# Performance work log

Hardware: AMD Instinct MI355X
Metric: run time of the kernel (lower is better)

The kernel has to match this reference:

```python
import jax, jax.numpy as jnp
import numpy as np

H, W = 300, 400            # grid_size
RES = 0.1                  # resolution (m/pixel)
X0, X1 = -20.0, 20.0       # x_range
Y0, Y1 = -10.0, 30.0       # y_range
Z0, Z1 = -3.0, 4.0         # z_range
MAX_INT = 255.0            # max_intensity
N_MAX = 128.0              # density_normalize
K_SAMPLES = 512            # >= max Bresenham steps inside grid (diag <= 400)


def _rasterize_polyline(pts_xy):
    """DDA line rasterization of an ego-frame polyline -> [H, W] binary grid.
    Matches the Bresenham + 3x3 stamp (width 2 or 3 -> half_w=1) of the original."""
    px = jnp.trunc((pts_xy[:, 0] - X0) / RES)  # int() truncation as in original
    py = jnp.trunc((pts_xy[:, 1] - Y0) / RES)
    p = jnp.stack([px, py], axis=-1)           # [N, 2] pixel coords (float)
    a, b = p[:-1], p[1:]                        # segment endpoints [S, 2]

    def inb(q):
        return (q[:, 0] >= 0) & (q[:, 0] < W) & (q[:, 1] >= 0) & (q[:, 1] < H)

    valid = inb(a) | inb(b)                     # draw if either endpoint in bounds
    lo = jnp.array([0.0, 0.0], jnp.float32)
    hi = jnp.array([W - 1.0, H - 1.0], jnp.float32)
    a = jnp.clip(a, lo, hi)
    b = jnp.clip(b, lo, hi)

    dmax = jnp.max(jnp.abs(b - a), axis=-1)     # [S] major-axis length in pixels
    k = jnp.arange(K_SAMPLES, dtype=jnp.float32)
    t = jnp.minimum(k[None, :], dmax[:, None]) / jnp.maximum(dmax[:, None], 1.0)
    pts = a[:, None, :] + t[..., None] * (b - a)[:, None, :]   # [S, K, 2]
    pix = jnp.round(pts).astype(jnp.int32)

    offs = jnp.arange(-1, 2)                    # half_w = width//2 = 1 -> 3x3 stamp
    xs = pix[..., 0][..., None, None] + offs[:, None]          # [S, K, 3, 1]
    ys = pix[..., 1][..., None, None] + offs[None, :]          # [S, K, 1, 3]
    xs, ys = jnp.broadcast_arrays(xs, ys)
    val = jnp.broadcast_to(valid.astype(jnp.float32)[:, None, None, None], xs.shape)
    # out-of-bounds stamped pixels are dropped, as in the original bounds check
    return jnp.zeros((H, W), jnp.float32).at[ys, xs].max(val, mode="drop")


def _rasterize_lidar(points):
    """[N,4] (x,y,z,intensity) -> [3,H,W] (height, mean intensity, log density)."""
    x, y, z, inten = points[:, 0], points[:, 1], points[:, 2], points[:, 3]
    mask = (x >= X0) & (x < X1) & (y >= Y0) & (y < Y1)
    px = jnp.clip(((x - X0) / RES).astype(jnp.int32), 0, W - 1)
    py = jnp.clip(((y - Y0) / RES).astype(jnp.int32), 0, H - 1)
    w = mask.astype(jnp.float32)
    neg_inf = jnp.float32(-jnp.inf)

    hmax = jnp.full((H, W), neg_inf, jnp.float32).at[py, px].max(
        jnp.where(mask, z, neg_inf))
    hmax = jnp.where(jnp.isneginf(hmax), 0.0, hmax)  # empty cells -> 0 BEFORE norm

    isum = jnp.zeros((H, W), jnp.float32).at[py, px].add(inten * w)
    cnt = jnp.zeros((H, W), jnp.float32).at[py, px].add(w)
    imean = jnp.where(cnt > 0, isum / jnp.maximum(cnt, 1.0), 0.0)

    h = jnp.clip((hmax - Z0) / (Z1 - Z0), 0.0, 1.0)
    i = jnp.clip(imean / MAX_INT, 0.0, 1.0)
    d = jnp.clip(jnp.log1p(cnt) / jnp.log(1.0 + N_MAX), 0.0, 1.0)
    return jnp.stack([h, i, d])


def setup_inputs() -> dict:
    key = jax.random.key(0)
    k1, k2 = jax.random.split(key)
    # LiDAR: 4M points, slightly wider than the ROI so ~some get filtered
    u = jax.random.uniform(k1, (4_000_000, 4), dtype=jnp.float32)
    lo = jnp.array([-25.0, -15.0, -3.0, 0.0], jnp.float32)
    hi = jnp.array([25.0, 35.0, 4.0, 255.0], jnp.float32)
    lidar_points = lo + u * (hi - lo)
    # trajectory: smooth forward path in ego frame
    ty = jnp.linspace(0.0, 25.0, 50, dtype=jnp.float32)
    tx = 2.0 * jnp.sin(0.3 * ty)
    trajectory = jnp.stack([tx, ty], axis=-1)
    # OSM polyline: random walk in world frame (ego at origin)
    steps = 0.5 * jax.random.normal(k2, (2000, 2), dtype=jnp.float32)
    osm_coords = jnp.cumsum(steps, axis=0) + jnp.array([0.0, 10.0], jnp.float32)
    ego_pose = jnp.zeros((3,), jnp.float32)
    return {"lidar_points": lidar_points, "trajectory": trajectory,
            "osm_coords": osm_coords, "ego_pose": ego_pose}


def reference(lidar_points, trajectory, osm_coords, ego_pose):
    lidar_bev = _rasterize_lidar(lidar_points)                 # [3,H,W]
    traj_bev = _rasterize_polyline(trajectory)[None]           # [1,H,W]
    # world -> ego for OSM coords
    cy, sy = jnp.cos(-ego_pose[2]), jnp.sin(-ego_pose[2])
    d = osm_coords - ego_pose[:2]
    osm_ego = jnp.stack([d[:, 0] * cy - d[:, 1] * sy,
                         d[:, 0] * sy + d[:, 1] * cy], axis=-1)
    map_bev = _rasterize_polyline(osm_ego)[None]               # [1,H,W]
    return jnp.concatenate([lidar_bev, traj_bev, map_bev], axis=0)  # [5,H,W]
```

## Files before the change

### kernel.cpp

```cpp
#include <hip/hip_runtime.h>
#include <math.h>

#define GH 300
#define GW 400
#define GHW (GH * GW)

#define TCOLS 25
#define TROWS 19
#define T_TILES (TCOLS * TROWS)
#define B1 1024
#define Q 16
#define CAP2 8192

__device__ __forceinline__ bool bin_point(float x, float y, int& px, int& py) {
    if (!(x >= -20.0f && x < 20.0f && y >= -10.0f && y < 30.0f)) return false;
    float qx = __fmul_rn(__fsub_rn(x, -20.0f), 10.0f);
    float qy = __fmul_rn(__fsub_rn(y, -10.0f), 10.0f);
    px = min(max((int)qx, 0), GW - 1);
    py = min(max((int)qy, 0), GH - 1);
    return true;
}

__device__ __forceinline__ void tile_prefix_wave0(const unsigned* src, unsigned* dst) {
    int lane = threadIdx.x;
    if (lane < 64) {
        unsigned run = 0;
        for (int c = 0; c < T_TILES; c += 64) {
            int idx = c + lane;
            unsigned v = (idx < T_TILES) ? src[idx] : 0u;
            unsigned orig = v;
#pragma unroll
            for (int d = 1; d < 64; d <<= 1) {
                unsigned u = __shfl_up(v, d, 64);
                if (lane >= d) v += u;
            }
            if (idx < T_TILES) dst[idx] = run + (v - orig);
            run += __shfl(v, 63, 64);
        }
        if (lane == 0) dst[T_TILES] = run;
    }
}

__device__ __forceinline__ bool make_record(float4 p, unsigned& rec, int& tile) {
    int px, py;
    if (!bin_point(p.x, p.y, px, py)) return false;
    tile = (py >> 4) * TCOLS + (px >> 4);
    int local = ((py & 15) << 4) | (px & 15);
    int z16 = min(max((int)rintf(__fmul_rn(__fadd_rn(p.z, 3.0f), 65535.0f / 7.0f)), 0), 65535);
    int i8 = min(max((int)rintf(p.w), 0), 255);
    rec = ((unsigned)z16 << 16) | ((unsigned)i8 << 8) | (unsigned)local;
    return true;
}

__global__ __launch_bounds__(256) void p1_kernel(const float4* __restrict__ pts, int n,
                                                 int per_block,
                                                 unsigned* __restrict__ staged,
                                                 unsigned* __restrict__ pref_t,
                                                 float* __restrict__ out) {
    __shared__ unsigned lbuf[256 * Q];
    __shared__ unsigned short ltile[256 * Q];
    __shared__ unsigned cnt[T_TILES];
    __shared__ unsigned pref[T_TILES + 1];
    __shared__ unsigned cur[T_TILES];
    for (int t = threadIdx.x; t < T_TILES; t += 256) cnt[t] = 0;
    float4* z4 = (float4*)(out + 3 * GHW);
    for (int j = blockIdx.x * 256 + (int)threadIdx.x; j < (2 * GHW) / 4; j += B1 * 256)
        z4[j] = make_float4(0.0f, 0.0f, 0.0f, 0.0f);
    __syncthreads();

    int start = blockIdx.x * per_block;
    int end = min(start + per_block, n);
    int nmine = 0;
    int i = start + (int)threadIdx.x;
    for (; i + 7 * 256 < end; i += 8 * 256) {
        float4 p[8];
#pragma unroll
        for (int j = 0; j < 8; ++j) p[j] = pts[i + j * 256];
#pragma unroll
        for (int j = 0; j < 8; ++j) {
            unsigned r;
            int tile;
            if (make_record(p[j], r, tile)) {
                lbuf[nmine * 256 + threadIdx.x] = r;
                ltile[nmine * 256 + threadIdx.x] = (unsigned short)tile;
                ++nmine;
                atomicAdd(&cnt[tile], 1u);
            }
        }
    }
    for (; i < end; i += 256) {
        unsigned r;
        int tile;
        if (make_record(pts[i], r, tile)) {
            lbuf[nmine * 256 + threadIdx.x] = r;
            ltile[nmine * 256 + threadIdx.x] = (unsigned short)tile;
            ++nmine;
            atomicAdd(&cnt[tile], 1u);
        }
    }
    __syncthreads();
    tile_prefix_wave0(cnt, pref);
    __syncthreads();
    for (int t = threadIdx.x; t < T_TILES; t += 256) cur[t] = pref[t];
    for (int t = threadIdx.x; t <= T_TILES; t += 256)
        pref_t[t * B1 + blockIdx.x] = pref[t];
    __syncthreads();
    size_t base = (size_t)blockIdx.x * (size_t)per_block;
    for (int j = 0; j < nmine; ++j) {
        unsigned r = lbuf[j * 256 + threadIdx.x];
        int tile = (int)ltile[j * 256 + threadIdx.x];
        unsigned pos = atomicAdd(&cur[tile], 1u);
        staged[base + pos] = r;
    }
}

__device__ void do_poly_segment(int seg, const float2* __restrict__ traj, int ntraj,
                                const float2* __restrict__ osm, int nosm,
                                const float* __restrict__ ego, float* __restrict__ out) {
    int ntseg = ntraj - 1;
    int noseg = nosm - 1;
    if (seg >= ntseg + noseg) return;
    const float2* pts;
    float* out_ch;
    bool use_ego;
    if (seg < ntseg) {
        pts = traj + seg;
        out_ch = out + 3 * GHW;
        use_ego = false;
    } else {
        pts = osm + (seg - ntseg);
        out_ch = out + 4 * GHW;
        use_ego = true;
    }
    float2 P0 = pts[0];
    float2 P1 = pts[1];
    if (use_ego) {
        float yaw = ego[2];
        float cy = cosf(-yaw), sy = sinf(-yaw);
        float ex = ego[0], ey = ego[1];
        float d0x = __fsub_rn(P0.x, ex), d0y = __fsub_rn(P0.y, ey);
        float d1x = __fsub_rn(P1.x, ex), d1y = __fsub_rn(P1.y, ey);
        P0.x = __fsub_rn(__fmul_rn(d0x, cy), __fmul_rn(d0y, sy));
        P0.y = __fadd_rn(__fmul_rn(d0x, sy), __fmul_rn(d0y, cy));
        P1.x = __fsub_rn(__fmul_rn(d1x, cy), __fmul_rn(d1y, sy));
        P1.y = __fadd_rn(__fmul_rn(d1x, sy), __fmul_rn(d1y, cy));
    }
    double ax = trunc(__ddiv_rn(__dadd_rn((double)P0.x, 20.0), 0.1));
    double ay = trunc(__ddiv_rn(__dadd_rn((double)P0.y, 10.0), 0.1));
    double bx = trunc(__ddiv_rn(__dadd_rn((double)P1.x, 20.0), 0.1));
    double by = trunc(__ddiv_rn(__dadd_rn((double)P1.y, 10.0), 0.1));
    bool inA = (ax >= 0.0) && (ax < (double)GW) && (ay >= 0.0) && (ay < (double)GH);
    bool inB = (bx >= 0.0) && (bx < (double)GW) && (by >= 0.0) && (by < (double)GH);
    if (!(inA || inB)) return;
    ax = fmin(fmax(ax, 0.0), (double)(GW - 1));
    ay = fmin(fmax(ay, 0.0), (double)(GH - 1));
    bx = fmin(fmax(bx, 0.0), (double)(GW - 1));
    by = fmin(fmax(by, 0.0), (double)(GH - 1));
    double dx = __dsub_rn(bx, ax);
    double dy = __dsub_rn(by, ay);
    double dmax = fmax(fabs(dx), fabs(dy));
    double denom = fmax(dmax, 1.0);
    int kmax = (int)dmax;
    for (int k = 0; k <= kmax; ++k) {
        double t = __ddiv_rn(fmin((double)k, dmax), denom);
        double ptx = __dadd_rn(ax, __dmul_rn(t, dx));
        double pty = __dadd_rn(ay, __dmul_rn(t, dy));
        int cx = (int)rint(ptx);
        int cc = (int)rint(pty);
#pragma unroll
        for (int oy = -1; oy <= 1; ++oy) {
#pragma unroll
            for (int ox = -1; ox <= 1; ++ox) {
                int xx = cx + ox;
                int yy = cc + oy;
                if (xx < 0) xx += GW;
                if (yy < 0) yy += GH;
                if (xx >= 0 && xx < GW && yy >= 0 && yy < GH) {
                    out_ch[yy * GW + xx] = 1.0f;
                }
            }
        }
    }
}

__global__ __launch_bounds__(1024) void p2_kernel(const unsigned* __restrict__ staged,
                                                  const unsigned* __restrict__ pref_t,
                                                  int per_block,
                                                  float* __restrict__ out,
                                                  const float2* __restrict__ traj, int ntraj,
                                                  const float2* __restrict__ osm, int nosm,
                                                  const float* __restrict__ ego) {
    if (blockIdx.x >= T_TILES) {
        int seg = (blockIdx.x - T_TILES) * 1024 + (int)threadIdx.x;
        do_poly_segment(seg, traj, ntraj, osm, nosm, ego, out);
        return;
    }
    __shared__ unsigned zmax[256];
    __shared__ unsigned long long ic[256];
    __shared__ unsigned cumB[B1 + 1];
    __shared__ unsigned addr_lds[CAP2];
    __shared__ unsigned wsum[16];
    int l = threadIdx.x;
    if (l < 256) {
        zmax[l] = 0;
        ic[l] = 0;
    }

    int bid = blockIdx.x;
    const int NX = 8;
    const int q = T_TILES / NX;
    const int r = T_TILES % NX;
    int xk = bid % NX;
    int jj = bid / NX;
    int t = (xk < r ? xk * (q + 1) : r * (q + 1) + (xk - r) * q) + jj;

    unsigned a0 = pref_t[t * B1 + l];
    unsigned a1 = pref_t[(t + 1) * B1 + l];
    unsigned c = a1 - a0;

    int lane = l & 63, wid = l >> 6;
    unsigned v = c;
#pragma unroll
    for (int d = 1; d < 64; d <<= 1) {
        unsigned u = __shfl_up(v, d, 64);
        if (lane >= d) v += u;
    }
    if (lane == 63) wsum[wid] = v;
    __syncthreads();
    if (l < 16) {
        unsigned wv = wsum[l];
        unsigned worig = wv;
#pragma unroll
        for (int d = 1; d < 16; d <<= 1) {
            unsigned u = __shfl_up(wv, d, 16);
            if (l >= d) wv += u;
        }
        wsum[l] = wv - worig;
    }
    __syncthreads();
    unsigned myBase = (v - c) + wsum[wid];
    cumB[l] = myBase;
    if (l == B1 - 1) cumB[B1] = myBase + c;
    __syncthreads();
    unsigned nrec = cumB[B1];
    unsigned myAddr0 = (unsigned)l * (unsigned)per_block + a0;

    for (unsigned b0 = 0; b0 < nrec; b0 += CAP2) {
        unsigned bh = min(b0 + CAP2, nrec);
        unsigned j0 = max(myBase, b0);
        unsigned j1 = min(myBase + c, bh);
        for (unsigned j = j0; j < j1; ++j)
            addr_lds[j - b0] = myAddr0 + (j - myBase);
        __syncthreads();
        unsigned nb = bh - b0;
        unsigned ad[8], rr[8];
        bool val[8];
#pragma unroll
        for (int i2 = 0; i2 < 8; ++i2) {
            unsigned ki = (unsigned)l + (unsigned)(i2 * 1024);
            val[i2] = ki < nb;
            ad[i2] = val[i2] ? addr_lds[ki] : 0u;
        }
#pragma unroll
        for (int i2 = 0; i2 < 8; ++i2) {
            if (val[i2]) rr[i2] = staged[ad[i2]];
        }
#pragma unroll
        for (int i2 = 0; i2 < 8; ++i2) {
            if (val[i2]) {
                unsigned r2 = rr[i2];
                int local = (int)(r2 & 255u);
                atomicMax(&zmax[local], r2 >> 16);
                atomicAdd(&ic[local], (1ull << 32) | ((r2 >> 8) & 255ull));
            }
        }
        __syncthreads();
    }

    if (l < 256) {
        unsigned zfin = zmax[l];
        unsigned long long v2 = ic[l];
        int trow = t / TCOLS, tcol = t % TCOLS;
        int gy = trow * 16 + (l >> 4);
        int gx = tcol * 16 + (l & 15);
        if (gy < GH) {
            const float inv7 = 1.0f / 7.0f;
            const float invlog129 = 1.0f / 4.8598124043616719e+00f;
            float h, ich, dd;
            if (v2 == 0) {
                h = fminf(fmaxf(__fmul_rn(3.0f, inv7), 0.0f), 1.0f);
                ich = 0.0f;
                dd = 0.0f;
            } else {
                unsigned cnt = (unsigned)(v2 >> 32);
                float sum8 = (float)(unsigned)(v2 & 0xFFFFFFFFull);
                h = fminf((float)zfin * (1.0f / 65535.0f), 1.0f);
                ich = fminf(__fdiv_rn(sum8, __fmul_rn((float)cnt, 255.0f)), 1.0f);
                dd = fminf(__fmul_rn(log1pf((float)cnt), invlog129), 1.0f);
            }
            int idx = gy * GW + gx;
            out[0 * GHW + idx] = h;
            out[1 * GHW + idx] = ich;
            out[2 * GHW + idx] = dd;
        }
    }
}

__global__ __launch_bounds__(256) void polylines_kernel(const float2* __restrict__ traj,
                                                        int ntraj,
                                                        const float2* __restrict__ osm, int nosm,
                                                        const float* __restrict__ ego,
                                                        float* __restrict__ out) {
    int seg = blockIdx.x * 256 + (int)threadIdx.x;
    do_poly_segment(seg, traj, ntraj, osm, nosm, ego, out);
}

__global__ __launch_bounds__(256) void init_kernel(float* __restrict__ out) {
    int i = blockIdx.x * blockDim.x + threadIdx.x;
    if (i < GHW) {
        out[0 * GHW + i] = -INFINITY;
        out[1 * GHW + i] = 0.0f;
        out[2 * GHW + i] = 0.0f;
        out[3 * GHW + i] = 0.0f;
        out[4 * GHW + i] = 0.0f;
    }
}

__device__ __forceinline__ void atomicMaxFloat(float* addr, float val) {
    if (val >= 0.0f) {
        atomicMax((int*)addr, __float_as_int(val));
    } else {
        atomicMin((unsigned int*)addr, (unsigned int)__float_as_int(val));
    }
}

__global__ __launch_bounds__(256) void lidar_kernel(const float4* __restrict__ pts, int n,
                                                    float* __restrict__ out) {
    int i = blockIdx.x * blockDim.x + threadIdx.x;
    if (i >= n) return;
    float4 p = pts[i];
    int px, py;
    if (!bin_point(p.x, p.y, px, py)) return;
    int idx = py * GW + px;
    atomicMaxFloat(&out[0 * GHW + idx], p.z);
    atomicAdd(&out[1 * GHW + idx], p.w);
    atomicAdd(&out[2 * GHW + idx], 1.0f);
}

__global__ __launch_bounds__(256) void finalize_kernel(float* __restrict__ out) {
    int i = blockIdx.x * blockDim.x + threadIdx.x;
    if (i >= GHW) return;
    float hm = out[0 * GHW + i];
    float isum = out[1 * GHW + i];
    float c = out[2 * GHW + i];
    if (hm == -INFINITY) hm = 0.0f;
    const float inv7 = 1.0f / 7.0f;
    const float inv255 = 1.0f / 255.0f;
    const float invlog129 = 1.0f / 4.8598124043616719e+00f;
    float h = fminf(fmaxf(__fmul_rn(__fadd_rn(hm, 3.0f), inv7), 0.0f), 1.0f);
    float im = (c > 0.0f) ? __fdiv_rn(isum, fmaxf(c, 1.0f)) : 0.0f;
    float ich = fminf(fmaxf(__fmul_rn(im, inv255), 0.0f), 1.0f);
    float dd = fminf(fmaxf(__fmul_rn(log1pf(c), invlog129), 0.0f), 1.0f);
    out[0 * GHW + i] = h;
    out[1 * GHW + i] = ich;
    out[2 * GHW + i] = dd;
}

extern "C" void kernel_launch(void* const* d_in, const int* in_sizes, int n_in,
                              void* d_out, int out_size, void* d_ws, size_t ws_size,
                              hipStream_t stream) {
    const float* lidar = (const float*)d_in[0];
    const float* traj = (const float*)d_in[1];
    const float* osm = (const float*)d_in[2];
    const float* ego = (const float*)d_in[3];
    float* out = (float*)d_out;

    int n_lidar = in_sizes[0] / 4;
    int n_traj = in_sizes[1] / 2;
    int n_osm = in_sizes[2] / 2;
    int nseg = (n_traj - 1) + (n_osm - 1);
    int npb = (nseg + 1023) / 1024;

    int per_block = (n_lidar + B1 - 1) / B1;
    size_t staged_bytes = (size_t)B1 * (size_t)per_block * 4;
    size_t pref_bytes = (size_t)(T_TILES + 1) * B1 * 4;
    size_t need = staged_bytes + pref_bytes;

    if (ws_size >= need && per_block <= 256 * Q) {
        char* w = (char*)d_ws;
        unsigned* staged = (unsigned*)w;
        unsigned* pref_t = (unsigned*)(w + staged_bytes);

        p1_kernel<<<B1, 256, 0, stream>>>((const float4*)lidar, n_lidar, per_block, staged,
                                          pref_t, out);
        p2_kernel<<<T_TILES + npb, 1024, 0, stream>>>(staged, pref_t, per_block, out,
                                                      (const float2*)traj, n_traj,
                                                      (const float2*)osm, n_osm, ego);
    } else {
        init_kernel<<<(GHW + 255) / 256, 256, 0, stream>>>(out);
        lidar_kernel<<<(n_lidar + 255) / 256, 256, 0, stream>>>((const float4*)lidar, n_lidar,
                                                                out);
        finalize_kernel<<<(GHW + 255) / 256, 256, 0, stream>>>(out);
        polylines_kernel<<<(nseg + 255) / 256, 256, 0, stream>>>((const float2*)traj, n_traj,
                                                                 (const float2*)osm, n_osm, ego,
                                                                 out);
    }
}
```

Measured before the change: 139.4 us.

## Load-balance polyline rasterization across threads via block scan and binary search

The polyline blocks previously gave each thread a whole segment and looped over every sample, so a few long segments left most lanes idle. Now each thread computes its segment's sample count, a block-wide exclusive scan assigns global sample indices, and threads pull individual samples found by binary search over the cumulative counts. Segment parameters are staged in shared memory, which is aliased with the tile-path buffers through one char array. This adds a scan, two barriers and a 10-step binary search per sample in exchange for balanced work across lanes.

```diff
diff --git a/kernel.cpp b/kernel.cpp
--- a/kernel.cpp
+++ b/kernel.cpp
@@ -11,6 +11,8 @@
 #define B1 1024
 #define Q 16
 #define CAP2 8192
+
+#define SMEM_BYTES 41056
 
 __device__ __forceinline__ bool bin_point(float x, float y, int& px, int& py) {
     if (!(x >= -20.0f && x < 20.0f && y >= -10.0f && y < 30.0f)) return false;
@@ -39,6 +41,29 @@
         }
         if (lane == 0) dst[T_TILES] = run;
     }
+}
+
+__device__ __forceinline__ unsigned block_scan_excl_1024(unsigned c, unsigned* wsum, int l) {
+    int lane = l & 63, wid = l >> 6;
+    unsigned v = c;
+#pragma unroll
+    for (int d = 1; d < 64; d <<= 1) {
+        unsigned u = __shfl_up(v, d, 64);
+        if (lane >= d) v += u;
+    }
+    if (lane == 63) wsum[wid] = v;
+    __syncthreads();
+    if (l < 16) {
+        unsigned wv = wsum[l], worig = wv;
+#pragma unroll
+        for (int d = 1; d < 16; d <<= 1) {
+            unsigned u = __shfl_up(wv, d, 16);
+            if (l >= d) wv += u;
+        }
+        wsum[l] = wv - worig;
+    }
+    __syncthreads();
+    return (v - c) + wsum[wid];
 }
 
 __device__ __forceinline__ bool make_record(float4 p, unsigned& rec, int& tile) {
@@ -190,17 +215,116 @@
                                                   const float2* __restrict__ traj, int ntraj,
                                                   const float2* __restrict__ osm, int nosm,
                                                   const float* __restrict__ ego) {
+    __shared__ char smem[SMEM_BYTES];
+    int l = threadIdx.x;
+
     if (blockIdx.x >= T_TILES) {
-        int seg = (blockIdx.x - T_TILES) * 1024 + (int)threadIdx.x;
-        do_poly_segment(seg, traj, ntraj, osm, nosm, ego, out);
+        double* ax_s = (double*)(smem);
+        double* ay_s = (double*)(smem + 8192);
+        double* dx_s = (double*)(smem + 16384);
+        double* dy_s = (double*)(smem + 24576);
+        unsigned* cum = (unsigned*)(smem + 32768);
+        unsigned* chan = (unsigned*)(smem + 36868);
+        unsigned* wsum = (unsigned*)(smem + 40964);
+
+        int pb = blockIdx.x - T_TILES;
+        int seg = pb * 1024 + l;
+        int ntseg = ntraj - 1;
+        int noseg = nosm - 1;
+        int nseg = ntseg + noseg;
+        unsigned jobs = 0;
+        if (seg < nseg) {
+            const float2* pts;
+            bool use_ego;
+            unsigned ch;
+            if (seg < ntseg) {
+                pts = traj + seg;
+                ch = 3u;
+                use_ego = false;
+            } else {
+                pts = osm + (seg - ntseg);
+                ch = 4u;
+                use_ego = true;
+            }
+            float2 P0 = pts[0];
+            float2 P1 = pts[1];
+            if (use_ego) {
+                float yaw = ego[2];
+                float cy = cosf(-yaw), sy = sinf(-yaw);
+                float ex = ego[0], ey = ego[1];
+                float d0x = __fsub_rn(P0.x, ex), d0y = __fsub_rn(P0.y, ey);
+                float d1x = __fsub_rn(P1.x, ex), d1y = __fsub_rn(P1.y, ey);
+                P0.x = __fsub_rn(__fmul_rn(d0x, cy), __fmul_rn(d0y, sy));
+                P0.y = __fadd_rn(__fmul_rn(d0x, sy), __fmul_rn(d0y, cy));
+                P1.x = __fsub_rn(__fmul_rn(d1x, cy), __fmul_rn(d1y, sy));
+                P1.y = __fadd_rn(__fmul_rn(d1x, sy), __fmul_rn(d1y, cy));
+            }
+            double ax = trunc(__ddiv_rn(__dadd_rn((double)P0.x, 20.0), 0.1));
+            double ay = trunc(__ddiv_rn(__dadd_rn((double)P0.y, 10.0), 0.1));
+            double bx = trunc(__ddiv_rn(__dadd_rn((double)P1.x, 20.0), 0.1));
+            double by = trunc(__ddiv_rn(__dadd_rn((double)P1.y, 10.0), 0.1));
+            bool inA = (ax >= 0.0) && (ax < (double)GW) && (ay >= 0.0) && (ay < (double)GH);
+            bool inB = (bx >= 0.0) && (bx < (double)GW) && (by >= 0.0) && (by < (double)GH);
+            if (inA || inB) {
+                ax = fmin(fmax(ax, 0.0), (double)(GW - 1));
+                ay = fmin(fmax(ay, 0.0), (double)(GH - 1));
+                bx = fmin(fmax(bx, 0.0), (double)(GW - 1));
+                by = fmin(fmax(by, 0.0), (double)(GH - 1));
+                double dx = __dsub_rn(bx, ax);
+                double dy = __dsub_rn(by, ay);
+                double dmax = fmax(fabs(dx), fabs(dy));
+                jobs = (unsigned)((int)dmax) + 1u;
+                ax_s[l] = ax;
+                ay_s[l] = ay;
+                dx_s[l] = dx;
+                dy_s[l] = dy;
+                chan[l] = ch;
+            }
+        }
+        unsigned excl = block_scan_excl_1024(jobs, wsum, l);
+        cum[l] = excl;
+        if (l == 1023) cum[1024] = excl + jobs;
+        __syncthreads();
+        unsigned tot = cum[1024];
+        for (unsigned j = l; j < tot; j += 1024) {
+            unsigned lo = 0, hi = 1024;
+#pragma unroll
+            for (int it = 0; it < 10; ++it) {
+                unsigned mid = (lo + hi) >> 1;
+                if (cum[mid] <= j) lo = mid; else hi = mid;
+            }
+            int k = (int)(j - cum[lo]);
+            double ax = ax_s[lo], ay = ay_s[lo], dx = dx_s[lo], dy = dy_s[lo];
+            double dmax = fmax(fabs(dx), fabs(dy));
+            double denom = fmax(dmax, 1.0);
+            double t = __ddiv_rn(fmin((double)k, dmax), denom);
+            double ptx = __dadd_rn(ax, __dmul_rn(t, dx));
+            double pty = __dadd_rn(ay, __dmul_rn(t, dy));
+            int cx = (int)rint(ptx);
+            int cc = (int)rint(pty);
+            float* out_ch = out + (size_t)chan[lo] * GHW;
+#pragma unroll
+            for (int oy = -1; oy <= 1; ++oy) {
+#pragma unroll
+                for (int ox = -1; ox <= 1; ++ox) {
+                    int xx = cx + ox;
+                    int yy = cc + oy;
+                    if (xx < 0) xx += GW;
+                    if (yy < 0) yy += GH;
+                    if (xx >= 0 && xx < GW && yy >= 0 && yy < GH) {
+                        out_ch[yy * GW + xx] = 1.0f;
+                    }
+                }
+            }
+        }
         return;
     }
-    __shared__ unsigned zmax[256];
-    __shared__ unsigned long long ic[256];
-    __shared__ unsigned cumB[B1 + 1];
-    __shared__ unsigned addr_lds[CAP2];
-    __shared__ unsigned wsum[16];
-    int l = threadIdx.x;
+
+    unsigned long long* ic = (unsigned long long*)(smem);
+    unsigned* addr_lds = (unsigned*)(smem + 2048);
+    unsigned* cumB = (unsigned*)(smem + 34816);
+    unsigned* zmax = (unsigned*)(smem + 38916);
+    unsigned* wsum = (unsigned*)(smem + 39940);
     if (l < 256) {
         zmax[l] = 0;
         ic[l] = 0;
@@ -217,28 +341,7 @@
     unsigned a0 = pref_t[t * B1 + l];
     unsigned a1 = pref_t[(t + 1) * B1 + l];
     unsigned c = a1 - a0;
-
-    int lane = l & 63, wid = l >> 6;
-    unsigned v = c;
-#pragma unroll
-    for (int d = 1; d < 64; d <<= 1) {
-        unsigned u = __shfl_up(v, d, 64);
-        if (lane >= d) v += u;
-    }
-    if (lane == 63) wsum[wid] = v;
-    __syncthreads();
-    if (l < 16) {
-        unsigned wv = wsum[l];
-        unsigned worig = wv;
-#pragma unroll
-        for (int d = 1; d < 16; d <<= 1) {
-            unsigned u = __shfl_up(wv, d, 16);
-            if (l >= d) wv += u;
-        }
-        wsum[l] = wv - worig;
-    }
-    __syncthreads();
-    unsigned myBase = (v - c) + wsum[wid];
+    unsigned myBase = block_scan_excl_1024(c, wsum, l);
     cumB[l] = myBase;
     if (l == B1 - 1) cumB[B1] = myBase + c;
     __syncthreads();
```

Result: faster. 130.9 us (-6.1%).
